# Optimization experiments

Hardware: AMD Instinct MI355X
Metric: run time of the kernel (lower is better)

Reference implementation:

```python
import jax, jax.numpy as jnp
import numpy as np

LR, AT, DSBETA, EPS_DS = 0.3, 0.9, 1e-4, 0.01


def setup_inputs() -> dict:
    key = jax.random.key(0)
    k1, k2, k3, k4, k5 = jax.random.split(key, 5)
    B, K, D = 8192, 4096, 512
    # 0.25 scale -> squared distances small enough that act_max straddles the 0.9 threshold
    return {
        "input": jax.random.normal(k1, (B, D), jnp.float32) * 0.25,
        "weights": jax.random.normal(k2, (K, D), jnp.float32) * 0.25,
        "moving_avg": jax.random.uniform(k3, (K, D), jnp.float32),
        "relevance": jax.random.uniform(k4, (K, D), jnp.float32),
        "node_control": jax.random.randint(k5, (K,), 0, 2).astype(jnp.float32),
    }


def _forward(input, weights, moving_avg, relevance, node_control):
    B, D = input.shape
    K = weights.shape[0]
    # activation: relevance-weighted pairwise sq-distance
    rel_sum = relevance.sum(1)                                   # [K]
    d = ((input ** 2).sum(1)[:, None] + (weights ** 2).sum(1)[None, :]
         - 2.0 * input @ weights.T)                              # [B,K]
    dw = d * (rel_sum / D)[None, :]
    dw = jnp.where(jnp.isnan(dw), 0.0, dw)
    act = rel_sum[None, :] / (rel_sum[None, :] + dw + 1e-7)      # [B,K]
    act_max = act.max(1)
    idx = jnp.argmax(act, 1)                                     # BMU per sample
    high = act_max >= AT                                         # [B]

    # ---- high-activation branch: segment-mean EMA update of winning nodes ----
    hi = high.astype(input.dtype)
    cnt = jax.ops.segment_sum(hi, idx, num_segments=K)           # [K]
    sums = jax.ops.segment_sum(input * hi[:, None], idx, num_segments=K)
    upd = cnt > 0                                                # nodes that won >=1 high sample
    mean_k = sums / jnp.where(upd, cnt, 1.0)[:, None]            # per-node mean sample
    dist_abs = jnp.abs(mean_k - weights)
    a = LR * DSBETA
    ma1 = jnp.where(upd[:, None], a * dist_abs + (1.0 - a) * moving_avg, moving_avg)
    mx = ma1.max(1, keepdims=True)
    mn = ma1.min(1, keepdims=True)
    av = ma1.mean(1, keepdims=True)
    rel_new = 1.0 / (1.0 + jnp.exp((ma1 - av) / (EPS_DS * (mx - mn))))
    rel1 = jnp.where(upd[:, None], rel_new, relevance)
    delta = LR * (mean_k - weights)
    w1 = jnp.where(upd[:, None], weights + delta, weights)
    nc1 = jnp.where(upd, 1.0, node_control)
    loss = (delta * upd[:, None]).sum() / B

    # ---- low-activation branch: add_node -> copy segment means into free slots ----
    lo = (~high).astype(input.dtype)
    cnt_l = jax.ops.segment_sum(lo, idx, num_segments=K)
    sums_l = jax.ops.segment_sum(input * lo[:, None], idx, num_segments=K)
    low_valid = cnt_l > 0
    low_mean = sums_l / jnp.where(low_valid, cnt_l, 1.0)[:, None]
    avail = nc1 == 0
    n_new = low_valid.sum()
    n_avail = avail.sum()
    n_create = jnp.minimum(n_new, n_avail)
    # torch.unique returns sorted node ids; stable argsort puts valid ids first ascending
    low_order = jnp.argsort(jnp.where(low_valid, 0, 1))          # [K]
    avail_order = jnp.argsort(jnp.where(avail, 0, 1))            # [K]
    r = jnp.arange(K)
    # add_node takes the LAST n_create new samples, fills FIRST n_create free slots
    src = low_order[jnp.clip(n_new - n_create + r, 0, K - 1)]
    vals = low_mean[src]                                         # [K,D]
    wm = r < n_create                                            # write mask per rank
    slot = avail_order                                           # permutation of [K]
    w2 = w1.at[slot].set(jnp.where(wm[:, None], vals, w1[slot]))
    ma2 = ma1.at[slot].set(jnp.where(wm[:, None], 0.0, ma1[slot]))
    rel2 = rel1.at[slot].set(jnp.where(wm[:, None], 1.0, rel1[slot]))
    nc2 = nc1.at[slot].set(jnp.where(wm, 1.0, nc1[slot]))

    state = jnp.stack([w2, ma2, rel2], axis=0)                   # [3,K,D]
    return loss, state, nc2


def reference(input, weights, moving_avg, relevance, node_control):
    return _forward(input, weights, moving_avg, relevance, node_control)
```

## Files before the change

### kernel.cpp

```cpp
#include <hip/hip_runtime.h>

typedef unsigned short ushort_t;
typedef unsigned int uint_t;
typedef __bf16 bf16x8 __attribute__((ext_vector_type(8)));
typedef float f32x4 __attribute__((ext_vector_type(4)));

#define BM 128
#define BN 128

static constexpr float LRC  = 0.3f;
static constexpr float AC   = (float)(0.3 * 1e-4);
static constexpr float OMAC = (float)(1.0 - 0.3 * 1e-4);
static constexpr float EPSC = 0.01f;
static constexpr float ATC  = 0.9f;
static constexpr float DELTA = 5e-4f;

__device__ __forceinline__ void gll16(const void* g, void* l) {
    __builtin_amdgcn_global_load_lds((__attribute__((address_space(1))) void*)g,
                                     (__attribute__((address_space(3))) void*)l,
                                     16, 0, 0);
}

__device__ __forceinline__ ushort_t f2bf_rne(float f) {
    uint_t u = __float_as_uint(f);
    uint_t r = u + 0x7fffu + ((u >> 16) & 1u);
    return (ushort_t)(r >> 16);
}

__global__ __launch_bounds__(128) void k_prep(
    const float* __restrict__ X, const float* __restrict__ W,
    const float* __restrict__ REL,
    ushort_t* __restrict__ Xh, ushort_t* __restrict__ Wh,
    float* __restrict__ xsq, float* __restrict__ wsq, float* __restrict__ rel_sum,
    int B, int D)
{
    int blk = blockIdx.x, t = threadIdx.x;
    bool isX = blk < B;
    int row = isX ? blk : blk - B;
    const float4* src = (const float4*)((isX ? X : W) + (size_t)row * D);
    const float4* rr  = isX ? nullptr : (const float4*)(REL + (size_t)row * D);
    ushort_t* H = isX ? Xh : Wh;
    float q = 0.f, r = 0.f;
    for (int i = t; i < (D >> 2); i += 128) {
        float4 v = src[i];
        if (!isX) { float4 rv = rr[i]; r += rv.x + rv.y + rv.z + rv.w; }
        float x[4] = {v.x, v.y, v.z, v.w};
        ushort_t h[4];
#pragma unroll
        for (int j = 0; j < 4; j++) { q += x[j] * x[j]; h[j] = f2bf_rne(x[j]); }
        ((ushort4*)H)[(size_t)row * (D >> 2) + i] = make_ushort4(h[0], h[1], h[2], h[3]);
    }
    __shared__ float s1[128], s2[128];
    s1[t] = q; s2[t] = r; __syncthreads();
    for (int off = 64; off > 0; off >>= 1) {
        if (t < off) { s1[t] += s1[t + off]; s2[t] += s2[t + off]; }
        __syncthreads();
    }
    if (t == 0) {
        if (isX) xsq[row] = s1[0];
        else { wsq[row] = s1[0]; rel_sum[row] = s2[0]; }
    }
}

__global__ __launch_bounds__(256, 2) void k_gemm_act(
    const ushort_t* __restrict__ Xh, const ushort_t* __restrict__ Wh,
    const float* __restrict__ xsq, const float* __restrict__ wsq,
    const float* __restrict__ rs,
    float* __restrict__ tmaxA, int* __restrict__ cntA,
    float* __restrict__ actsA, int* __restrict__ idxsA,
    int K, int D)
{
    __shared__ char smem[26112];

    const int tid = threadIdx.x;
    const int wave = tid >> 6, lane = tid & 63;
    const int nk = K / BN;
    const int bx = blockIdx.x % nk, by = blockIdx.x / nk;
    const int b0 = by * BM, k0 = bx * BN;

    const int srow = wave * 32 + (lane >> 2);
    const int schunk = ((lane & 3) - (lane >> 3)) & 3;
    const int scol = schunk * 8;
    const size_t gx = (size_t)(b0 + srow) * D + scol;
    const size_t gw = (size_t)(k0 + srow) * D + scol;
    const size_t c1 = (size_t)16 * D;
    char* lb = smem + wave * 2048;

    const int wm = wave >> 1, wn = wave & 1;
    const int l15 = lane & 15, quad = lane >> 4;
    const int roff = (l15 * 4 + ((quad + (l15 >> 1)) & 3)) * 16;
    const int aoff = (wm * 4) * 1024 + roff;
    const int boff = (wn * 4) * 1024 + roff;

    f32x4 acc[4][4];
#pragma unroll
    for (int i = 0; i < 4; i++)
#pragma unroll
        for (int j = 0; j < 4; j++) acc[i][j] = (f32x4){0.f, 0.f, 0.f, 0.f};

    for (int kd = 0; kd < D; kd += 32) {
        gll16(Xh + gx + kd,      lb + 0);
        gll16(Xh + gx + c1 + kd, lb + 1024);
        gll16(Wh + gw + kd,      lb + 8192);
        gll16(Wh + gw + c1 + kd, lb + 8192 + 1024);
        __syncthreads();

        bf16x8 ah[4], bh[4];
#pragma unroll
        for (int t = 0; t < 4; t++) {
            ah[t] = *(const bf16x8*)(smem + 0    + aoff + t * 1024);
            bh[t] = *(const bf16x8*)(smem + 8192 + boff + t * 1024);
        }
#pragma unroll
        for (int j = 0; j < 4; j++)
#pragma unroll
            for (int i = 0; i < 4; i++)
                acc[i][j] = __builtin_amdgcn_mfma_f32_16x16x32_bf16(ah[i], bh[j], acc[i][j], 0, 0, 0);
        __syncthreads();
    }

    float rsv[4], wqv[4];
#pragma unroll
    for (int tn = 0; tn < 4; tn++) {
        int c = k0 + wn * 64 + tn * 16 + l15;
        rsv[tn] = rs[c]; wqv[tn] = wsq[c];
    }
    const float invD = 1.f / (float)D;
    float* redM    = (float*)smem;
    float* tmaxrow = (float*)(smem + 16896);
    int*   cntL    = (int*)(smem + 17408);
    float* lsActs  = (float*)(smem + 17920);
    int*   lsIdx   = (int*)(smem + 22016);

#pragma unroll
    for (int tm = 0; tm < 4; tm++) {
#pragma unroll
        for (int r = 0; r < 4; r++) {
            int rowl = wm * 64 + tm * 16 + quad * 4 + r;
            float xq = xsq[b0 + rowl];
            float m = -1e30f;
#pragma unroll
            for (int tn = 0; tn < 4; tn++) {
                float dd = (xq + wqv[tn]) - 2.f * acc[tm][tn][r];
                float dw = dd * (rsv[tn] * invD);
                if (dw != dw) dw = 0.f;
                float act = rsv[tn] / ((rsv[tn] + dw) + 1e-7f);
                m = fmaxf(m, act);
            }
            redM[rowl * 33 + wn * 16 + l15] = m;
        }
    }
    __syncthreads();
    if (tid < BM) {
        float m = -1e30f;
#pragma unroll
        for (int t2 = 0; t2 < 32; t2++) m = fmaxf(m, redM[tid * 33 + t2]);
        tmaxrow[tid] = m;
        cntL[tid] = 0;
    }
    __syncthreads();
#pragma unroll
    for (int tm = 0; tm < 4; tm++) {
#pragma unroll
        for (int r = 0; r < 4; r++) {
            int rowl = wm * 64 + tm * 16 + quad * 4 + r;
            float xq = xsq[b0 + rowl];
            float thr = tmaxrow[rowl] - DELTA;
#pragma unroll
            for (int tn = 0; tn < 4; tn++) {
                float dd = (xq + wqv[tn]) - 2.f * acc[tm][tn][r];
                float dw = dd * (rsv[tn] * invD);
                if (dw != dw) dw = 0.f;
                float act = rsv[tn] / ((rsv[tn] + dw) + 1e-7f);
                if (act >= thr) {
                    int pos = atomicAdd(&cntL[rowl], 1);
                    if (pos < 8) {
                        lsActs[rowl * 8 + pos] = act;
                        lsIdx[rowl * 8 + pos]  = k0 + wn * 64 + tn * 16 + l15;
                    }
                }
            }
        }
    }
    __syncthreads();
    if (tid < BM) {
        size_t base = (size_t)(b0 + tid) * nk + bx;
        tmaxA[base] = tmaxrow[tid];
        int c = cntL[tid];
        cntA[base] = c;
        int cc = c < 8 ? c : 8;
        for (int s = 0; s < cc; s++) {
            actsA[base * 8 + s] = lsActs[tid * 8 + s];
            idxsA[base * 8 + s] = lsIdx[tid * 8 + s];
        }
    }
}

__global__ __launch_bounds__(64) void k_refine(
    const float* __restrict__ X, const float* __restrict__ W,
    const float* __restrict__ xsq, const float* __restrict__ wsq,
    const float* __restrict__ rs,
    const float* __restrict__ tmaxA, const int* __restrict__ cntA,
    const float* __restrict__ actsA, const int* __restrict__ idxsA,
    int nk, int* __restrict__ cnt, int* __restrict__ cnt_l,
    int* __restrict__ idxb, int* __restrict__ rankb, int* __restrict__ highb,
    int K, int D)
{
    int b = blockIdx.x, ln = threadIdx.x;
    const float4* xp = (const float4*)(X + (size_t)b * D + ln * 8);
    float4 xa = xp[0], xb = xp[1];
    float xr[8] = {xa.x, xa.y, xa.z, xa.w, xb.x, xb.y, xb.z, xb.w};
    float xq = xsq[b];
    const float invD = 1.f / (float)D;

    float tmax = (ln < nk) ? tmaxA[(size_t)b * nk + ln] : -1e30f;
    int   tcnt = (ln < nk) ? cntA[(size_t)b * nk + ln] : 0;
    float M = tmax;
#pragma unroll
    for (int o = 32; o > 0; o >>= 1) M = fmaxf(M, __shfl_xor(M, o));
    float thr = M - DELTA;

    float best = -1e30f; int bidx = 0x7fffffff;

    auto exact_upd = [&](int idx) {
        const float* wr = W + (size_t)idx * D + ln * 8;
        float p = 0.f;
#pragma unroll
        for (int j = 0; j < 8; j++) p = fmaf(xr[j], wr[j], p);
#pragma unroll
        for (int o = 32; o > 0; o >>= 1) p += __shfl_xor(p, o);
        float rsv = rs[idx];
        float dd = (xq + wsq[idx]) - 2.f * p;
        float dw = dd * (rsv * invD);
        if (dw != dw) dw = 0.f;
        float act = rsv / ((rsv + dw) + 1e-7f);
        if (act > best || (act == best && idx < bidx)) { best = act; bidx = idx; }
    };

    for (int t = 0; t < nk; t++) {
        float tm = __shfl(tmax, t);
        int   tc = __shfl(tcnt, t);
        if (tm < thr) continue;
        if (tc <= 8) {
            size_t base = ((size_t)b * nk + t) * 8;
            for (int s = 0; s < tc; s++) {
                float aact = actsA[base + s];
                if (aact < thr) continue;
                exact_upd(idxsA[base + s]);
            }
        } else {
            for (int k2 = t * BN; k2 < t * BN + BN; k2++) exact_upd(k2);
        }
    }

    if (ln == 0) {
        int hi = (best >= ATC) ? 1 : 0;
        int rank = atomicAdd((hi ? cnt : cnt_l) + bidx, 1);
        idxb[b] = bidx; rankb[b] = rank; highb[b] = hi;
    }
}

__global__ __launch_bounds__(1024) void k_offsets(
    const int* __restrict__ cnt, const int* __restrict__ cnt_l,
    const float* __restrict__ NC,
    int* __restrict__ offs_h, int* __restrict__ offs_l,
    int* __restrict__ low_ids, int* __restrict__ avail_ids,
    int* __restrict__ scal, int K)
{
    __shared__ int sA[1024], sB[1024];
    int t = threadIdx.x;
    int per = (K + 1023) / 1024;
    int base = t * per;
    int ch[8], cl[8]; int sh = 0, sl = 0;
    for (int j = 0; j < per; j++) {
        int k = base + j;
        int a = (k < K) ? cnt[k] : 0;
        int b = (k < K) ? cnt_l[k] : 0;
        ch[j] = a; cl[j] = b; sh += a; sl += b;
    }
    sA[t] = sh; sB[t] = sl; __syncthreads();
    for (int off = 1; off < 1024; off <<= 1) {
        int vA = (t >= off) ? sA[t - off] : 0;
        int vB = (t >= off) ? sB[t - off] : 0;
        __syncthreads();
        sA[t] += vA; sB[t] += vB;
        __syncthreads();
    }
    int eh = sA[t] - sh, el = sB[t] - sl;
    for (int j = 0; j < per; j++) {
        int k = base + j;
        if (k < K) { offs_h[k] = eh; offs_l[k] = el; }
        eh += ch[j]; el += cl[j];
    }
    __syncthreads();
    int lv[8], av[8]; int cL = 0, cA = 0;
    for (int j = 0; j < per; j++) {
        int k = base + j;
        int l = 0, a = 0;
        if (k < K) {
            l = (cl[j] > 0) ? 1 : 0;
            float nc1 = (ch[j] > 0) ? 1.f : NC[k];
            a = (nc1 == 0.f) ? 1 : 0;
        }
        lv[j] = l; av[j] = a; cL += l; cA += a;
    }
    sA[t] = cL; sB[t] = cA; __syncthreads();
    for (int off = 1; off < 1024; off <<= 1) {
        int vA = (t >= off) ? sA[t - off] : 0;
        int vB = (t >= off) ? sB[t - off] : 0;
        __syncthreads();
        sA[t] += vA; sB[t] += vB;
        __syncthreads();
    }
    int totL = sA[1023], totA = sB[1023];
    int eL = sA[t] - cL, eA = sB[t] - cA;
    for (int j = 0; j < per; j++) {
        if (lv[j]) low_ids[eL++] = base + j;
        if (av[j]) avail_ids[eA++] = base + j;
    }
    if (t == 0) {
        scal[0] = totL;
        scal[1] = totA;
        scal[2] = (totL < totA) ? totL : totA;
    }
}

__global__ __launch_bounds__(256) void k_scatter(
    const int* __restrict__ idxb, const int* __restrict__ rankb,
    const int* __restrict__ highb,
    const int* __restrict__ offs_h, const int* __restrict__ offs_l,
    int* __restrict__ list_h, int* __restrict__ list_l, int B)
{
    int b = blockIdx.x * 256 + threadIdx.x;
    if (b >= B) return;
    int node = idxb[b];
    if (highb[b]) list_h[offs_h[node] + rankb[b]] = b;
    else          list_l[offs_l[node] + rankb[b]] = b;
}

__global__ __launch_bounds__(256) void k_high_update(
    const float* __restrict__ X,
    const float* __restrict__ W, const float* __restrict__ MA,
    const float* __restrict__ REL, const float* __restrict__ NC,
    const int* __restrict__ cnt, const int* __restrict__ offs_h,
    const int* __restrict__ list_h,
    float* __restrict__ outW, float* __restrict__ outMA,
    float* __restrict__ outREL, float* __restrict__ outNC,
    float* __restrict__ outLoss, int D, float invB)
{
    int k = blockIdx.x, t = threadIdx.x;
    size_t ro = (size_t)k * D;
    int n = cnt[k];
    int t2 = t + 256;
    __shared__ float rbuf[12];
    if (n > 0) {
        float s0 = 0.f, s1 = 0.f;
        int base = offs_h[k];
        for (int i = 0; i < n; i++) {
            int b = list_h[base + i];
            const float* xr = X + (size_t)b * D;
            s0 += xr[t]; s1 += xr[t2];
        }
        float fn = (float)n;
        float mean0 = s0 / fn, mean1 = s1 / fn;
        float w0 = W[ro + t],  w1 = W[ro + t2];
        float a0 = MA[ro + t], a1 = MA[ro + t2];
        float m0 = AC * fabsf(mean0 - w0) + OMAC * a0;
        float m1 = AC * fabsf(mean1 - w1) + OMAC * a1;

        float vmax = fmaxf(m0, m1), vmin = fminf(m0, m1), vsum = m0 + m1;
#pragma unroll
        for (int o = 1; o < 64; o <<= 1) {
            vmax = fmaxf(vmax, __shfl_xor(vmax, o));
            vmin = fminf(vmin, __shfl_xor(vmin, o));
            vsum += __shfl_xor(vsum, o);
        }
        int wv = t >> 6, ln = t & 63;
        if (ln == 0) { rbuf[wv] = vmax; rbuf[4 + wv] = vmin; rbuf[8 + wv] = vsum; }
        __syncthreads();
        float mx = fmaxf(fmaxf(rbuf[0], rbuf[1]), fmaxf(rbuf[2], rbuf[3]));
        float mn = fminf(fminf(rbuf[4], rbuf[5]), fminf(rbuf[6], rbuf[7]));
        float av = (rbuf[8] + rbuf[9] + rbuf[10] + rbuf[11]) / (float)D;

        float scale = EPSC * (mx - mn);
        float r0 = 1.f / (1.f + expf((m0 - av) / scale));
        float r1 = 1.f / (1.f + expf((m1 - av) / scale));
        float d0 = LRC * (mean0 - w0), d1 = LRC * (mean1 - w1);

        outW[ro + t]  = w0 + d0;  outW[ro + t2]  = w1 + d1;
        outMA[ro + t] = m0;       outMA[ro + t2] = m1;
        outREL[ro + t] = r0;      outREL[ro + t2] = r1;

        float ls = d0 + d1;
#pragma unroll
        for (int o = 1; o < 64; o <<= 1) ls += __shfl_xor(ls, o);
        __syncthreads();
        if (ln == 0) rbuf[wv] = ls;
        __syncthreads();
        if (t == 0) {
            atomicAdd(outLoss, (rbuf[0] + rbuf[1] + rbuf[2] + rbuf[3]) * invB);
            outNC[k] = 1.f;
        }
    } else {
        outW[ro + t]  = W[ro + t];   outW[ro + t2]  = W[ro + t2];
        outMA[ro + t] = MA[ro + t];  outMA[ro + t2] = MA[ro + t2];
        outREL[ro + t] = REL[ro + t]; outREL[ro + t2] = REL[ro + t2];
        if (t == 0) outNC[k] = NC[k];
    }
}

__global__ __launch_bounds__(256) void k_addnode(
    const float* __restrict__ X,
    const int* __restrict__ cnt_l, const int* __restrict__ offs_l,
    const int* __restrict__ list_l,
    const int* __restrict__ low_ids, const int* __restrict__ avail_ids,
    const int* __restrict__ scal,
    float* __restrict__ outW, float* __restrict__ outMA,
    float* __restrict__ outREL, float* __restrict__ outNC, int D)
{
    int r = blockIdx.x;
    int n_create = scal[2], n_new = scal[0];
    if (r >= n_create) return;
    int slot = avail_ids[r];
    int src  = low_ids[n_new - n_create + r];
    int n = cnt_l[src];
    int t = threadIdx.x, t2 = t + 256;
    float s0 = 0.f, s1 = 0.f;
    int base = offs_l[src];
    for (int i = 0; i < n; i++) {
        int b = list_l[base + i];
        const float* xr = X + (size_t)b * D;
        s0 += xr[t]; s1 += xr[t2];
    }
    float fn = (float)n;
    size_t to = (size_t)slot * D;
    outW[to + t]  = s0 / fn;  outW[to + t2]  = s1 / fn;
    outMA[to + t] = 0.f;      outMA[to + t2] = 0.f;
    outREL[to + t] = 1.f;     outREL[to + t2] = 1.f;
    if (t == 0) outNC[slot] = 1.f;
}

extern "C" void kernel_launch(void* const* d_in, const int* in_sizes, int n_in,
                              void* d_out, int out_size, void* d_ws, size_t ws_size,
                              hipStream_t stream) {
    const float* X   = (const float*)d_in[0];
    const float* W   = (const float*)d_in[1];
    const float* MA  = (const float*)d_in[2];
    const float* REL = (const float*)d_in[3];
    const float* NC  = (const float*)d_in[4];

    const int K = in_sizes[4];
    const int D = in_sizes[1] / K;
    const int B = in_sizes[0] / D;
    const int NKT = K / BN;
    const size_t KD = (size_t)K * D;
    const size_t BD = (size_t)B * D;

    float* out = (float*)d_out;
    float* outLoss = out;
    float* outW   = out + 1;
    float* outMA  = out + 1 + KD;
    float* outREL = out + 1 + 2 * KD;
    float* outNC  = out + 1 + 3 * KD;

    float* wsf = (float*)d_ws;
    size_t off = 0;
    ushort_t* Xh = (ushort_t*)(wsf + off); off += BD / 2;
    ushort_t* Wh = (ushort_t*)(wsf + off); off += KD / 2;
    float* rel_sum = wsf + off; off += K;
    float* wsq     = wsf + off; off += K;
    float* xsq     = wsf + off; off += B;
    float* tmaxA   = wsf + off; off += (size_t)B * NKT;
    int*   cntA    = (int*)(wsf + off); off += (size_t)B * NKT;
    float* actsA   = wsf + off; off += (size_t)B * NKT * 8;
    int*   idxsA   = (int*)(wsf + off); off += (size_t)B * NKT * 8;
    int*   idxb    = (int*)(wsf + off); off += B;
    int*   rankb   = (int*)(wsf + off); off += B;
    int*   highb   = (int*)(wsf + off); off += B;
    int*   list_h  = (int*)(wsf + off); off += B;
    int*   list_l  = (int*)(wsf + off); off += B;
    int*   offs_h  = (int*)(wsf + off); off += K;
    int*   offs_l  = (int*)(wsf + off); off += K;
    int*   low_ids   = (int*)(wsf + off); off += K;
    int*   avail_ids = (int*)(wsf + off); off += K;
    int*   scal    = (int*)(wsf + off); off += 16;
    int*   cnt     = (int*)(wsf + off); off += K;
    int*   cnt_l   = (int*)(wsf + off); off += K;

    hipMemsetAsync(cnt, 0, 2 * (size_t)K * sizeof(int), stream);
    hipMemsetAsync(outLoss, 0, sizeof(float), stream);

    k_prep<<<B + K, 128, 0, stream>>>(X, W, REL, Xh, Wh, xsq, wsq, rel_sum, B, D);
    k_gemm_act<<<(B / BM) * (K / BN), 256, 0, stream>>>(Xh, Wh, xsq, wsq, rel_sum,
                                                        tmaxA, cntA, actsA, idxsA,
                                                        K, D);
    k_refine<<<B, 64, 0, stream>>>(X, W, xsq, wsq, rel_sum,
                                   tmaxA, cntA, actsA, idxsA, NKT,
                                   cnt, cnt_l, idxb, rankb, highb, K, D);
    k_offsets<<<1, 1024, 0, stream>>>(cnt, cnt_l, NC, offs_h, offs_l,
                                      low_ids, avail_ids, scal, K);
    k_scatter<<<(B + 255) / 256, 256, 0, stream>>>(idxb, rankb, highb,
                                                   offs_h, offs_l,
                                                   list_h, list_l, B);
    k_high_update<<<K, 256, 0, stream>>>(X, W, MA, REL, NC, cnt, offs_h, list_h,
                                         outW, outMA, outREL, outNC, outLoss,
                                         D, 1.f / (float)B);
    k_addnode<<<K, 256, 0, stream>>>(X, cnt_l, offs_l, list_l,
                                     low_ids, avail_ids, scal,
                                     outW, outMA, outREL, outNC, D);
}
```

Baseline: 265.8 us.

## Simplify activation epilogue algebraically and fuse add-node into final update kernel

```diff
diff --git a/kernel.cpp b/kernel.cpp
--- a/kernel.cpp
+++ b/kernel.cpp
@@ -70,7 +70,7 @@
     float* __restrict__ actsA, int* __restrict__ idxsA,
     int K, int D)
 {
-    __shared__ char smem[26112];
+    __shared__ char smem[26624];
 
     const int tid = threadIdx.x;
     const int wave = tid >> 6, lane = tid & 63;
@@ -119,18 +119,21 @@
         __syncthreads();
     }
 
-    float rsv[4], wqv[4];
+    float rsv[4], wqv[4], epsors[4];
 #pragma unroll
     for (int tn = 0; tn < 4; tn++) {
         int c = k0 + wn * 64 + tn * 16 + l15;
-        rsv[tn] = rs[c]; wqv[tn] = wsq[c];
+        float rv = rs[c];
+        rsv[tn] = rv; wqv[tn] = wsq[c];
+        epsors[tn] = 1e-7f / rv;
     }
     const float invD = 1.f / (float)D;
     float* redM    = (float*)smem;
     float* tmaxrow = (float*)(smem + 16896);
-    int*   cntL    = (int*)(smem + 17408);
-    float* lsActs  = (float*)(smem + 17920);
-    int*   lsIdx   = (int*)(smem + 22016);
+    float* thrqrow = (float*)(smem + 17408);
+    int*   cntL    = (int*)(smem + 17920);
+    float* lsActs  = (float*)(smem + 18432);
+    int*   lsIdx   = (int*)(smem + 22528);
 
 #pragma unroll
     for (int tm = 0; tm < 4; tm++) {
@@ -138,24 +141,25 @@
         for (int r = 0; r < 4; r++) {
             int rowl = wm * 64 + tm * 16 + quad * 4 + r;
             float xq = xsq[b0 + rowl];
-            float m = -1e30f;
+            float qmin = 1e30f;
 #pragma unroll
             for (int tn = 0; tn < 4; tn++) {
                 float dd = (xq + wqv[tn]) - 2.f * acc[tm][tn][r];
-                float dw = dd * (rsv[tn] * invD);
-                if (dw != dw) dw = 0.f;
-                float act = rsv[tn] / ((rsv[tn] + dw) + 1e-7f);
-                m = fmaxf(m, act);
+                float q = dd * invD + epsors[tn];
+                acc[tm][tn][r] = q;
+                qmin = fminf(qmin, q);
             }
-            redM[rowl * 33 + wn * 16 + l15] = m;
+            redM[rowl * 33 + wn * 16 + l15] = qmin;
         }
     }
     __syncthreads();
     if (tid < BM) {
-        float m = -1e30f;
-#pragma unroll
-        for (int t2 = 0; t2 < 32; t2++) m = fmaxf(m, redM[tid * 33 + t2]);
-        tmaxrow[tid] = m;
+        float qm = 1e30f;
+#pragma unroll
+        for (int t2 = 0; t2 < 32; t2++) qm = fminf(qm, redM[tid * 33 + t2]);
+        float tmax = 1.f / (1.f + qm);
+        tmaxrow[tid] = tmax;
+        thrqrow[tid] = 1.f / (tmax - DELTA) - 1.f;
         cntL[tid] = 0;
     }
     __syncthreads();
@@ -164,18 +168,14 @@
 #pragma unroll
         for (int r = 0; r < 4; r++) {
             int rowl = wm * 64 + tm * 16 + quad * 4 + r;
-            float xq = xsq[b0 + rowl];
-            float thr = tmaxrow[rowl] - DELTA;
+            float tq = thrqrow[rowl];
 #pragma unroll
             for (int tn = 0; tn < 4; tn++) {
-                float dd = (xq + wqv[tn]) - 2.f * acc[tm][tn][r];
-                float dw = dd * (rsv[tn] * invD);
-                if (dw != dw) dw = 0.f;
-                float act = rsv[tn] / ((rsv[tn] + dw) + 1e-7f);
-                if (act >= thr) {
+                float q = acc[tm][tn][r];
+                if (q <= tq) {
                     int pos = atomicAdd(&cntL[rowl], 1);
                     if (pos < 8) {
-                        lsActs[rowl * 8 + pos] = act;
+                        lsActs[rowl * 8 + pos] = 1.f / (1.f + q);
                         lsIdx[rowl * 8 + pos]  = k0 + wn * 64 + tn * 16 + l15;
                     }
                 }
@@ -264,10 +264,10 @@
     const int* __restrict__ cnt, const int* __restrict__ cnt_l,
     const float* __restrict__ NC,
     int* __restrict__ offs_h, int* __restrict__ offs_l,
-    int* __restrict__ low_ids, int* __restrict__ avail_ids,
-    int* __restrict__ scal, int K)
+    int* __restrict__ slot_src, int K)
 {
     __shared__ int sA[1024], sB[1024];
+    __shared__ int lowL[4096], availL[4096];
     int t = threadIdx.x;
     int per = (K + 1023) / 1024;
     int base = t * per;
@@ -315,14 +315,17 @@
     int totL = sA[1023], totA = sB[1023];
     int eL = sA[t] - cL, eA = sB[t] - cA;
     for (int j = 0; j < per; j++) {
-        if (lv[j]) low_ids[eL++] = base + j;
-        if (av[j]) avail_ids[eA++] = base + j;
-    }
-    if (t == 0) {
-        scal[0] = totL;
-        scal[1] = totA;
-        scal[2] = (totL < totA) ? totL : totA;
-    }
+        if (lv[j]) lowL[eL++] = base + j;
+        if (av[j]) availL[eA++] = base + j;
+    }
+    for (int j = 0; j < per; j++) {
+        int k = base + j;
+        if (k < K) slot_src[k] = -1;
+    }
+    __syncthreads();
+    int n_create = (totL < totA) ? totL : totA;
+    for (int r = t; r < n_create; r += 1024)
+        slot_src[availL[r]] = lowL[totL - n_create + r];
 }
 
 __global__ __launch_bounds__(256) void k_scatter(
@@ -338,22 +341,39 @@
     else          list_l[offs_l[node] + rankb[b]] = b;
 }
 
-__global__ __launch_bounds__(256) void k_high_update(
+__global__ __launch_bounds__(256) void k_final(
     const float* __restrict__ X,
     const float* __restrict__ W, const float* __restrict__ MA,
     const float* __restrict__ REL, const float* __restrict__ NC,
     const int* __restrict__ cnt, const int* __restrict__ offs_h,
     const int* __restrict__ list_h,
+    const int* __restrict__ cnt_l, const int* __restrict__ offs_l,
+    const int* __restrict__ list_l, const int* __restrict__ slot_src,
     float* __restrict__ outW, float* __restrict__ outMA,
     float* __restrict__ outREL, float* __restrict__ outNC,
     float* __restrict__ outLoss, int D, float invB)
 {
     int k = blockIdx.x, t = threadIdx.x;
     size_t ro = (size_t)k * D;
+    int t2 = t + 256;
+    int src = slot_src[k];
     int n = cnt[k];
-    int t2 = t + 256;
     __shared__ float rbuf[12];
-    if (n > 0) {
+    if (src >= 0) {
+        int m = cnt_l[src];
+        int base = offs_l[src];
+        float s0 = 0.f, s1 = 0.f;
+        for (int i = 0; i < m; i++) {
+            int b = list_l[base + i];
+            const float* xr = X + (size_t)b * D;
+            s0 += xr[t]; s1 += xr[t2];
+        }
+        float fm = (float)m;
+        outW[ro + t]  = s0 / fm; outW[ro + t2]  = s1 / fm;
+        outMA[ro + t] = 0.f;     outMA[ro + t2] = 0.f;
+        outREL[ro + t] = 1.f;    outREL[ro + t2] = 1.f;
+        if (t == 0) outNC[k] = 1.f;
+    } else if (n > 0) {
         float s0 = 0.f, s1 = 0.f;
         int base = offs_h[k];
         for (int i = 0; i < n; i++) {
@@ -407,37 +427,6 @@
         outREL[ro + t] = REL[ro + t]; outREL[ro + t2] = REL[ro + t2];
         if (t == 0) outNC[k] = NC[k];
     }
-}
-
-__global__ __launch_bounds__(256) void k_addnode(
-    const float* __restrict__ X,
-    const int* __restrict__ cnt_l, const int* __restrict__ offs_l,
-    const int* __restrict__ list_l,
-    const int* __restrict__ low_ids, const int* __restrict__ avail_ids,
-    const int* __restrict__ scal,
-    float* __restrict__ outW, float* __restrict__ outMA,
-    float* __restrict__ outREL, float* __restrict__ outNC, int D)
-{
-    int r = blockIdx.x;
-    int n_create = scal[2], n_new = scal[0];
-    if (r >= n_create) return;
-    int slot = avail_ids[r];
-    int src  = low_ids[n_new - n_create + r];
-    int n = cnt_l[src];
-    int t = threadIdx.x, t2 = t + 256;
-    float s0 = 0.f, s1 = 0.f;
-    int base = offs_l[src];
-    for (int i = 0; i < n; i++) {
-        int b = list_l[base + i];
-        const float* xr = X + (size_t)b * D;
-        s0 += xr[t]; s1 += xr[t2];
-    }
-    float fn = (float)n;
-    size_t to = (size_t)slot * D;
-    outW[to + t]  = s0 / fn;  outW[to + t2]  = s1 / fn;
-    outMA[to + t] = 0.f;      outMA[to + t2] = 0.f;
-    outREL[to + t] = 1.f;     outREL[to + t2] = 1.f;
-    if (t == 0) outNC[slot] = 1.f;
 }
 
 extern "C" void kernel_launch(void* const* d_in, const int* in_sizes, int n_in,
@@ -481,9 +470,7 @@
     int*   list_l  = (int*)(wsf + off); off += B;
     int*   offs_h  = (int*)(wsf + off); off += K;
     int*   offs_l  = (int*)(wsf + off); off += K;
-    int*   low_ids   = (int*)(wsf + off); off += K;
-    int*   avail_ids = (int*)(wsf + off); off += K;
-    int*   scal    = (int*)(wsf + off); off += 16;
+    int*   slot_src = (int*)(wsf + off); off += K;
     int*   cnt     = (int*)(wsf + off); off += K;
     int*   cnt_l   = (int*)(wsf + off); off += K;
 
@@ -498,14 +485,12 @@
                                    tmaxA, cntA, actsA, idxsA, NKT,
                                    cnt, cnt_l, idxb, rankb, highb, K, D);
     k_offsets<<<1, 1024, 0, stream>>>(cnt, cnt_l, NC, offs_h, offs_l,
-                                      low_ids, avail_ids, scal, K);
+                                      slot_src, K);
     k_scatter<<<(B + 255) / 256, 256, 0, stream>>>(idxb, rankb, highb,
                                                    offs_h, offs_l,
                                                    list_h, list_l, B);
-    k_high_update<<<K, 256, 0, stream>>>(X, W, MA, REL, NC, cnt, offs_h, list_h,
-                                         outW, outMA, outREL, outNC, outLoss,
-                                         D, 1.f / (float)B);
-    k_addnode<<<K, 256, 0, stream>>>(X, cnt_l, offs_l, list_l,
-                                     low_ids, avail_ids, scal,
-                                     outW, outMA, outREL, outNC, D);
-}
+    k_final<<<K, 256, 0, stream>>>(X, W, MA, REL, NC, cnt, offs_h, list_h,
+                                   cnt_l, offs_l, list_l, slot_src,
+                                   outW, outMA, outREL, outNC, outLoss,
+                                   D, 1.f / (float)B);
+}
```

Result: faster. 251.6 us (-5.3%).
